# Kernel optimization log

Measured on AMD Instinct MI355X. Metric: run time of the kernel, lower is better.

The kernel has to match this reference:

```python
import jax, jax.numpy as jnp
import numpy as np

N_NODES = 100000
N_EDGES = 3200000
N_GRAPHS = 256
HID = 128


def _glorot(key, shape):
    fan_in = shape[1]
    return jax.random.normal(key, shape, dtype=jnp.float32) / jnp.sqrt(jnp.float32(fan_in))


def setup_inputs() -> dict:
    key = jax.random.key(0)
    ks = jax.random.split(key, 16)
    x = jax.random.normal(ks[0], (N_NODES, 50), dtype=jnp.float32)
    edge_index = jax.random.randint(ks[1], (2, N_EDGES), 0, N_NODES, dtype=jnp.int32)
    batch = jnp.sort(jax.random.randint(ks[2], (N_NODES,), 0, N_GRAPHS, dtype=jnp.int32))
    d1, d2, d3 = HID, HID * 2, HID * 4
    params = {
        'w1l': _glorot(ks[3], (d1, 50)), 'b1': jnp.zeros((d1,), jnp.float32), 'w1r': _glorot(ks[4], (d1, 50)),
        'w2l': _glorot(ks[5], (d2, d1)), 'b2': jnp.zeros((d2,), jnp.float32), 'w2r': _glorot(ks[6], (d2, d1)),
        'w3l': _glorot(ks[7], (d3, d2)), 'b3': jnp.zeros((d3,), jnp.float32), 'w3r': _glorot(ks[8], (d3, d2)),
        'fc1_w': _glorot(ks[9], (d2, d3)), 'fc1_b': jnp.zeros((d2,), jnp.float32),
        'fc2_w': _glorot(ks[10], (d1, d2)), 'fc2_b': jnp.zeros((d1,), jnp.float32),
        'cls_w': _glorot(ks[11], (15, d1)), 'cls_b': jnp.zeros((15,), jnp.float32),
    }
    return {'x': x, 'edge_index': edge_index, 'batch': batch, **params}


def _sage_conv(x, src, dst, wl, b, wr):
    # PyG SAGEConv (mean aggr): out = lin_l(mean_j x_j) + lin_r(x_i)
    agg = jax.ops.segment_sum(x[src], dst, num_segments=N_NODES)
    deg = jax.ops.segment_sum(jnp.ones((src.shape[0],), x.dtype), dst, num_segments=N_NODES)
    agg = agg / jnp.maximum(deg, 1.0)[:, None]
    return agg @ wl.T + b + x @ wr.T


def reference(x, edge_index, batch,
              w1l, b1, w1r, w2l, b2, w2r, w3l, b3, w3r,
              fc1_w, fc1_b, fc2_w, fc2_b, cls_w, cls_b):
    src, dst = edge_index[0], edge_index[1]
    # eval mode: dropout is identity
    h = jax.nn.leaky_relu(_sage_conv(x, src, dst, w1l, b1, w1r), negative_slope=0.01)
    h = jax.nn.relu(_sage_conv(h, src, dst, w2l, b2, w2r))
    h = jax.nn.relu(_sage_conv(h, src, dst, w3l, b3, w3r))
    # global mean pool over graphs
    pooled = jax.ops.segment_sum(h, batch, num_segments=N_GRAPHS)
    cnt = jax.ops.segment_sum(jnp.ones((h.shape[0],), h.dtype), batch, num_segments=N_GRAPHS)
    pooled = pooled / jnp.maximum(cnt, 1.0)[:, None]
    z = jax.nn.relu(pooled @ fc1_w.T + fc1_b)
    z = jax.nn.relu(z @ fc2_w.T + fc2_b)
    return z @ cls_w.T + cls_b
```

## Files before the change

kernel.cpp:

```cpp
#include <hip/hip_runtime.h>
#include <hip/hip_bf16.h>

#define N_NODES 100000
#define N_EDGES 3200000
#define N_GRAPHS 256
#define CAP 80
#define NB 1563
#define NPB 64
#define PBLK 512
#define EPB 6250

typedef __hip_bfloat16 bf16;
using f32x4  = __attribute__((ext_vector_type(4))) float;
using f32x2  = __attribute__((ext_vector_type(2))) float;
using short8 = __attribute__((ext_vector_type(8))) short;

__global__ __launch_bounds__(256) void p1_count(const int* __restrict__ dst,
                                                int* __restrict__ bcount) {
    __shared__ int hist[NB];
    int i = blockIdx.x;
    for (int b = threadIdx.x; b < NB; b += 256) hist[b] = 0;
    __syncthreads();
    int base = i * EPB;
    for (int j = threadIdx.x; j < EPB; j += 256)
        atomicAdd(&hist[dst[base + j] >> 6], 1);
    __syncthreads();
    for (int b = threadIdx.x; b < NB; b += 256) bcount[(size_t)b * PBLK + i] = hist[b];
}

__global__ __launch_bounds__(512) void p2a_total(const int* __restrict__ bcount,
                                                 int* __restrict__ btotal) {
    __shared__ int red[512];
    int b = blockIdx.x;
    red[threadIdx.x] = bcount[(size_t)b * PBLK + threadIdx.x];
    __syncthreads();
    for (int off = 256; off > 0; off >>= 1) {
        if (threadIdx.x < off) red[threadIdx.x] += red[threadIdx.x + off];
        __syncthreads();
    }
    if (threadIdx.x == 0) btotal[b] = red[0];
}

__global__ __launch_bounds__(1024) void p2b_scan(const int* __restrict__ btotal,
                                                 int* __restrict__ bbase) {
    __shared__ int buf[1024];
    __shared__ int carry;
    if (threadIdx.x == 0) carry = 0;
    __syncthreads();
    for (int t = 0; t < NB; t += 1024) {
        int i = t + threadIdx.x;
        int v = (i < NB) ? btotal[i] : 0;
        buf[threadIdx.x] = v;
        __syncthreads();
        for (int off = 1; off < 1024; off <<= 1) {
            int tv = (threadIdx.x >= off) ? buf[threadIdx.x - off] : 0;
            __syncthreads();
            buf[threadIdx.x] += tv;
            __syncthreads();
        }
        if (i < NB) bbase[i] = carry + buf[threadIdx.x] - v;
        __syncthreads();
        if (threadIdx.x == 0) carry += buf[1023];
        __syncthreads();
    }
    if (threadIdx.x == 0) bbase[NB] = carry;
}

__global__ __launch_bounds__(512) void p2c_off(const int* __restrict__ bcount,
                                               const int* __restrict__ bbase,
                                               int* __restrict__ off) {
    __shared__ int buf[512];
    int b = blockIdx.x;
    int v = bcount[(size_t)b * PBLK + threadIdx.x];
    buf[threadIdx.x] = v;
    __syncthreads();
    for (int o = 1; o < 512; o <<= 1) {
        int t = (threadIdx.x >= o) ? buf[threadIdx.x - o] : 0;
        __syncthreads();
        buf[threadIdx.x] += t;
        __syncthreads();
    }
    off[(size_t)threadIdx.x * NB + b] = bbase[b] + buf[threadIdx.x] - v;
}

__global__ __launch_bounds__(256) void p3_scatter(const int* __restrict__ src,
                                                  const int* __restrict__ dst,
                                                  const int* __restrict__ off,
                                                  unsigned int* __restrict__ ebuf) {
    __shared__ int loff[NB];
    int i = blockIdx.x;
    for (int b = threadIdx.x; b < NB; b += 256) loff[b] = off[(size_t)i * NB + b];
    __syncthreads();
    int base = i * EPB;
    for (int j = threadIdx.x; j < EPB; j += 256) {
        int d = dst[base + j];
        int p = atomicAdd(&loff[d >> 6], 1);
        ebuf[p] = ((unsigned)src[base + j] << 6) | (unsigned)(d & 63);
    }
}

__global__ __launch_bounds__(256) void p4_csr(const unsigned int* __restrict__ ebuf,
                                              const int* __restrict__ bbase,
                                              int* __restrict__ cols, int* __restrict__ cnt,
                                              float* __restrict__ invdeg) {
    __shared__ int lcnt[NPB];
    int b = blockIdx.x;
    if (threadIdx.x < NPB) lcnt[threadIdx.x] = 0;
    __syncthreads();
    int s = bbase[b], e = bbase[b + 1];
    int n0 = b * NPB;
    for (int j = s + threadIdx.x; j < e; j += 256) {
        unsigned int p = ebuf[j];
        int dl = p & 63;
        int r = atomicAdd(&lcnt[dl], 1);
        if (r < CAP) cols[(size_t)(n0 + dl) * CAP + r] = (int)(p >> 6);
    }
    __syncthreads();
    if (threadIdx.x < NPB) {
        int n = n0 + threadIdx.x;
        if (n < N_NODES) {
            int c = lcnt[threadIdx.x];
            cnt[n] = c;
            invdeg[n] = 1.0f / fmaxf((float)c, 1.0f);
        }
    }
}

__global__ void xprep_kernel(const float* __restrict__ x, bf16* __restrict__ xb) {
    int t = blockIdx.x * blockDim.x + threadIdx.x;
    if (t >= N_NODES * 64) return;
    int n = t >> 6, f = t & 63;
    xb[t] = __float2bfloat16(f < 50 ? x[(size_t)n * 50 + f] : 0.f);
}

__device__ __forceinline__ void wcvt(const float* __restrict__ s, bf16* __restrict__ d,
                                     int Din, int Kp, int lt) {
    int o = lt / Kp, kk = lt % Kp;
    d[lt] = __float2bfloat16(kk < Din ? s[(size_t)o * Din + kk] : 0.f);
}

__global__ void wprep_all_kernel(const float* w1l, const float* w1r,
                                 const float* w2l, const float* w2r,
                                 const float* w3l, const float* w3r,
                                 bf16* w1l_b, bf16* w1r_b, bf16* w2l_b, bf16* w2r_b,
                                 bf16* w3l_b, bf16* w3r_b) {
    int t = blockIdx.x * blockDim.x + threadIdx.x;
    if      (t < 8192)   wcvt(w1l, w1l_b, 50, 64, t);
    else if (t < 16384)  wcvt(w1r, w1r_b, 50, 64, t - 8192);
    else if (t < 49152)  wcvt(w2l, w2l_b, 128, 128, t - 16384);
    else if (t < 81920)  wcvt(w2r, w2r_b, 128, 128, t - 49152);
    else if (t < 212992) wcvt(w3l, w3l_b, 256, 256, t - 81920);
    else if (t < 344064) wcvt(w3r, w3r_b, 256, 256, t - 212992);
}

template <int D>
__global__ void aggv_kernel(const bf16* __restrict__ h, const int* __restrict__ cnt,
                            const int* __restrict__ cols, const float* __restrict__ invdeg,
                            bf16* __restrict__ AG) {
    constexpr int L = D / 8;
    int n = blockIdx.x * (256 / L) + threadIdx.x / L;
    int lane = threadIdx.x % L;
    if (n >= N_NODES) return;
    const int* cp = cols + (size_t)n * CAP;
    int deg = min(cnt[n], CAP);
    float acc[8] = {};
    auto accum = [&](uint4 v) {
        const unsigned short* u = (const unsigned short*)&v;
#pragma unroll
        for (int i = 0; i < 8; ++i) {
            union { unsigned int ui; float f; } cv;
            cv.ui = ((unsigned int)u[i]) << 16;
            acc[i] += cv.f;
        }
    };
    int j = 0;
    for (; j + 4 <= deg; j += 4) {
        int c0 = cp[j], c1 = cp[j + 1], c2 = cp[j + 2], c3 = cp[j + 3];
        uint4 v0 = *(const uint4*)&h[(size_t)c0 * D + lane * 8];
        uint4 v1 = *(const uint4*)&h[(size_t)c1 * D + lane * 8];
        uint4 v2 = *(const uint4*)&h[(size_t)c2 * D + lane * 8];
        uint4 v3 = *(const uint4*)&h[(size_t)c3 * D + lane * 8];
        accum(v0); accum(v1); accum(v2); accum(v3);
    }
    for (; j < deg; ++j) accum(*(const uint4*)&h[(size_t)cp[j] * D + lane * 8]);
    float inv = invdeg[n];
    union { uint4 u; bf16 h8[8]; } o;
#pragma unroll
    for (int i = 0; i < 8; ++i) o.h8[i] = __float2bfloat16(acc[i] * inv);
    *(uint4*)&AG[(size_t)n * D + lane * 8] = o.u;
}

template <int D>
__global__ void aggv8_kernel(const unsigned char* __restrict__ h8,
                             const int* __restrict__ cnt,
                             const int* __restrict__ cols, const float* __restrict__ invdeg,
                             bf16* __restrict__ AG) {
    constexpr int L = D / 8;
    int n = blockIdx.x * (256 / L) + threadIdx.x / L;
    int lane = threadIdx.x % L;
    if (n >= N_NODES) return;
    const int* cp = cols + (size_t)n * CAP;
    int deg = min(cnt[n], CAP);
    float acc[8] = {};
    auto accum = [&](uint2 v) {
        f32x2 a0 = __builtin_amdgcn_cvt_pk_f32_fp8(v.x, false);
        f32x2 a1 = __builtin_amdgcn_cvt_pk_f32_fp8(v.x, true);
        f32x2 a2 = __builtin_amdgcn_cvt_pk_f32_fp8(v.y, false);
        f32x2 a3 = __builtin_amdgcn_cvt_pk_f32_fp8(v.y, true);
        acc[0] += a0[0]; acc[1] += a0[1]; acc[2] += a1[0]; acc[3] += a1[1];
        acc[4] += a2[0]; acc[5] += a2[1]; acc[6] += a3[0]; acc[7] += a3[1];
    };
    int j = 0;
    for (; j + 8 <= deg; j += 8) {
        uint2 v[8];
#pragma unroll
        for (int q = 0; q < 8; ++q)
            v[q] = *(const uint2*)&h8[(size_t)cp[j + q] * D + lane * 8];
#pragma unroll
        for (int q = 0; q < 8; ++q) accum(v[q]);
    }
    for (; j < deg; ++j) accum(*(const uint2*)&h8[(size_t)cp[j] * D + lane * 8]);
    float inv = invdeg[n];
    union { uint4 u; bf16 hb[8]; } o;
#pragma unroll
    for (int i = 0; i < 8; ++i) o.hb[i] = __float2bfloat16(acc[i] * inv);
    *(uint4*)&AG[(size_t)n * D + lane * 8] = o.u;
}

template <int ACT, int POOL, int OUT8>
__global__ __launch_bounds__(256) void glds_gemm(
        const bf16* __restrict__ A1, const bf16* __restrict__ A2, int Kh,
        const bf16* __restrict__ B1, const bf16* __restrict__ B2,
        const float* __restrict__ bias, bf16* __restrict__ out,
        unsigned char* __restrict__ out8,
        int M, int Dout,
        const int* __restrict__ batch, float* __restrict__ pooled) {
    __shared__ alignas(16) bf16 As[2][128][32];
    __shared__ alignas(16) bf16 Bs[2][128][32];
    __shared__ int sbatch[128];

    const int tid = threadIdx.x;
    const int n0 = blockIdx.y * 128;
    const int o0 = blockIdx.x * 128;

    if (POOL && tid < 128) {
        int n = n0 + tid;
        sbatch[tid] = (n < M) ? batch[n] : -1;
    }

    const int lane = tid & 63;
    const int w = tid >> 6;
    const int wr = w >> 1, wc = w & 1;
    const int lr = lane & 15, hi = lane >> 4;
    const int l4 = lane >> 2;
    const int kc8 = (lane & 3) * 8;

    f32x4 acc[4][4] = {};

    auto stage = [&](int buf, int k0) {
        const bf16* Ap;
        const bf16* Bp;
        int kk;
        if (k0 < Kh) { Ap = A1; Bp = B1; kk = k0; }
        else         { Ap = A2; Bp = B2; kk = k0 - Kh; }
#pragma unroll
        for (int c = 0; c < 2; ++c) {
            int rl = w * 32 + c * 16 + l4;
            size_t ga = (size_t)min(n0 + rl, M - 1) * (size_t)Kh + kk + kc8;
            __builtin_amdgcn_global_load_lds(
                (const __attribute__((address_space(1))) void*)(Ap + ga),
                (__attribute__((address_space(3))) void*)&As[buf][w * 32 + c * 16][0], 16, 0, 0);
            size_t gb = (size_t)(o0 + rl) * (size_t)Kh + kk + kc8;
            __builtin_amdgcn_global_load_lds(
                (const __attribute__((address_space(1))) void*)(Bp + gb),
                (__attribute__((address_space(3))) void*)&Bs[buf][w * 32 + c * 16][0], 16, 0, 0);
        }
    };

    const int nt = (2 * Kh) / 32;
    stage(0, 0);
    asm volatile("s_waitcnt vmcnt(0)\n\ts_barrier" ::: "memory");

    int cur = 0;
    for (int t = 0; t < nt; ++t) {
        if (t + 1 < nt) stage(cur ^ 1, (t + 1) * 32);

        short8 af[4], bfr[4];
#pragma unroll
        for (int m = 0; m < 4; ++m)
            af[m] = *(const short8*)&As[cur][wr * 64 + m * 16 + lr][hi * 8];
#pragma unroll
        for (int n = 0; n < 4; ++n)
            bfr[n] = *(const short8*)&Bs[cur][wc * 64 + n * 16 + lr][hi * 8];
#pragma unroll
        for (int m = 0; m < 4; ++m)
#pragma unroll
            for (int n = 0; n < 4; ++n)
                acc[m][n] = __builtin_amdgcn_mfma_f32_16x16x32_bf16(af[m], bfr[n], acc[m][n], 0, 0, 0);

        if (t + 1 < nt)
            asm volatile("s_waitcnt vmcnt(0)\n\ts_barrier" ::: "memory");
        cur ^= 1;
    }

    float bias_v[4];
#pragma unroll
    for (int n = 0; n < 4; ++n) bias_v[n] = bias[o0 + wc * 64 + n * 16 + lr];

    if (!POOL) {
#pragma unroll
        for (int m = 0; m < 4; ++m) {
#pragma unroll
            for (int j = 0; j < 4; ++j) {
                int row = n0 + wr * 64 + m * 16 + hi * 4 + j;
                if (row < M) {
#pragma unroll
                    for (int n = 0; n < 4; ++n) {
                        int col = o0 + wc * 64 + n * 16 + lr;
                        float s = acc[m][n][j] + bias_v[n];
                        if (ACT == 0) s = (s >= 0.f) ? s : 0.01f * s;
                        else          s = fmaxf(s, 0.f);
                        out[(size_t)row * Dout + col] = __float2bfloat16(s);
                        if (OUT8) {
                            int p = __builtin_amdgcn_cvt_pk_fp8_f32(s, s, 0, false);
                            out8[(size_t)row * Dout + col] = (unsigned char)(p & 0xff);
                        }
                    }
                }
            }
        }
    } else {
        int lastv = min(127, M - 1 - n0);
        int gmin = sbatch[0], gmax = sbatch[lastv];
        for (int g = gmin; g <= gmax; ++g) {
            float s[4] = {0.f, 0.f, 0.f, 0.f};
#pragma unroll
            for (int m = 0; m < 4; ++m) {
#pragma unroll
                for (int j = 0; j < 4; ++j) {
                    int rl = wr * 64 + m * 16 + hi * 4 + j;
                    if (sbatch[rl] == g) {
#pragma unroll
                        for (int n = 0; n < 4; ++n)
                            s[n] += fmaxf(acc[m][n][j] + bias_v[n], 0.f);
                    }
                }
            }
#pragma unroll
            for (int n = 0; n < 4; ++n) {
                float v = s[n];
                v += __shfl_xor(v, 16, 64);
                v += __shfl_xor(v, 32, 64);
                if (hi == 0)
                    atomicAdd(&pooled[(size_t)g * 512 + o0 + wc * 64 + n * 16 + lr], v);
            }
        }
    }
}

__global__ void bounds_kernel(const int* __restrict__ batch, int* __restrict__ gstart) {
    int g = blockIdx.x * blockDim.x + threadIdx.x;
    if (g > N_GRAPHS) return;
    int lo = 0, hi = N_NODES;
    while (lo < hi) {
        int mid = (lo + hi) >> 1;
        if (batch[mid] < g) lo = mid + 1;
        else hi = mid;
    }
    gstart[g] = lo;
}

__global__ void pool_finalize(float* __restrict__ pooled, const int* __restrict__ gstart) {
    int g = blockIdx.x;
    int f = threadIdx.x;
    float cnt = fmaxf((float)(gstart[g + 1] - gstart[g]), 1.0f);
    pooled[(size_t)g * 512 + f] /= cnt;
}

template <int ACT>
__global__ void mlp_kernel(const float* __restrict__ in, const float* __restrict__ w,
                           const float* __restrict__ b, float* __restrict__ out,
                           int M, int K, int O) {
    int t = blockIdx.x * blockDim.x + threadIdx.x;
    if (t >= M * O) return;
    int m = t / O, o = t % O;
    const float* ip = in + (size_t)m * K;
    const float* wp = w + (size_t)o * K;
    float s = 0.f;
    for (int k = 0; k < K; ++k) s += ip[k] * wp[k];
    s += b[o];
    if (ACT) s = fmaxf(s, 0.f);
    out[(size_t)m * O + o] = s;
}

extern "C" void kernel_launch(void* const* d_in, const int* in_sizes, int n_in,
                              void* d_out, int out_size, void* d_ws, size_t ws_size,
                              hipStream_t stream) {
    const float* x     = (const float*)d_in[0];
    const int*   ei    = (const int*)d_in[1];
    const int*   batch = (const int*)d_in[2];
    const float* w1l = (const float*)d_in[3];
    const float* b1  = (const float*)d_in[4];
    const float* w1r = (const float*)d_in[5];
    const float* w2l = (const float*)d_in[6];
    const float* b2  = (const float*)d_in[7];
    const float* w2r = (const float*)d_in[8];
    const float* w3l = (const float*)d_in[9];
    const float* b3  = (const float*)d_in[10];
    const float* w3r = (const float*)d_in[11];
    const float* fc1_w = (const float*)d_in[12];
    const float* fc1_b = (const float*)d_in[13];
    const float* fc2_w = (const float*)d_in[14];
    const float* fc2_b = (const float*)d_in[15];
    const float* cls_w = (const float*)d_in[16];
    const float* cls_b = (const float*)d_in[17];
    float* out = (float*)d_out;

    const int* src = ei;
    const int* dst = ei + N_EDGES;

    char* wsp = (char*)d_ws;
    size_t used = 0;
    auto alloc = [&](size_t bytes) {
        char* p = wsp + used;
        used += (bytes + 255) & ~(size_t)255;
        return p;
    };
    int*   cnt    = (int*)alloc((size_t)N_NODES * 4);
    int*   cols   = (int*)alloc((size_t)N_NODES * CAP * 4);
    float* invdeg = (float*)alloc((size_t)N_NODES * 4);
    int*   gstart = (int*)alloc((size_t)(N_GRAPHS + 1) * 4);
    bf16*  xb     = (bf16*)alloc((size_t)N_NODES * 64 * 2);
    char*  R      = alloc((size_t)N_NODES * 256 * 2);
    bf16*  AG     = (bf16*)R;
    bf16*  h1     = (bf16*)(R + (size_t)N_NODES * 128 * 2);
    bf16*  h2     = (bf16*)alloc((size_t)N_NODES * 256 * 2);
    unsigned char* h1_8 = (unsigned char*)alloc((size_t)N_NODES * 128);
    unsigned char* h2_8 = (unsigned char*)alloc((size_t)N_NODES * 256);
    bf16*  w1l_b  = (bf16*)alloc(128 * 64 * 2);
    bf16*  w1r_b  = (bf16*)alloc(128 * 64 * 2);
    bf16*  w2l_b  = (bf16*)alloc(256 * 128 * 2);
    bf16*  w2r_b  = (bf16*)alloc(256 * 128 * 2);
    bf16*  w3l_b  = (bf16*)alloc(512 * 256 * 2);
    bf16*  w3r_b  = (bf16*)alloc(512 * 256 * 2);
    float* pooled = (float*)alloc((size_t)N_GRAPHS * 512 * 4);
    float* z1     = (float*)alloc((size_t)N_GRAPHS * 256 * 4);
    float* z2     = (float*)alloc((size_t)N_GRAPHS * 128 * 4);

    int* bcount = (int*)h1_8;
    int* btotal = bcount + (size_t)NB * PBLK;
    int* bbase  = btotal + NB;
    int* off    = bbase + NB + 1;
    unsigned int* ebuf = (unsigned int*)h2;

    if (ws_size < used) return;

    p1_count<<<PBLK, 256, 0, stream>>>(dst, bcount);
    p2a_total<<<NB, 512, 0, stream>>>(bcount, btotal);
    p2b_scan<<<1, 1024, 0, stream>>>(btotal, bbase);
    p2c_off<<<NB, 512, 0, stream>>>(bcount, bbase, off);
    p3_scatter<<<PBLK, 256, 0, stream>>>(src, dst, off, ebuf);
    p4_csr<<<NB, 256, 0, stream>>>(ebuf, bbase, cols, cnt, invdeg);
    bounds_kernel<<<2, 160, 0, stream>>>(batch, gstart);

    xprep_kernel<<<(N_NODES * 64 + 255) / 256, 256, 0, stream>>>(x, xb);
    wprep_all_kernel<<<(344064 + 255) / 256, 256, 0, stream>>>(
        w1l, w1r, w2l, w2r, w3l, w3r, w1l_b, w1r_b, w2l_b, w2r_b, w3l_b, w3r_b);

    const int MB = (N_NODES + 127) / 128;

    aggv_kernel<64><<<(N_NODES * 8 + 255) / 256, 256, 0, stream>>>(xb, cnt, cols, invdeg, AG);
    glds_gemm<0, 0, 1><<<dim3(1, MB), 256, 0, stream>>>(
        AG, xb, 64, w1l_b, w1r_b, b1, h1, h1_8, N_NODES, 128, nullptr, nullptr);

    aggv8_kernel<128><<<(N_NODES * 16 + 255) / 256, 256, 0, stream>>>(
        h1_8, cnt, cols, invdeg, AG);
    glds_gemm<1, 0, 1><<<dim3(2, MB), 256, 0, stream>>>(
        AG, h1, 128, w2l_b, w2r_b, b2, h2, h2_8, N_NODES, 256, nullptr, nullptr);

    aggv8_kernel<256><<<(N_NODES * 32 + 255) / 256, 256, 0, stream>>>(
        h2_8, cnt, cols, invdeg, AG);
    hipMemsetAsync(pooled, 0, (size_t)N_GRAPHS * 512 * 4, stream);
    glds_gemm<1, 1, 0><<<dim3(4, MB), 256, 0, stream>>>(
        AG, h2, 256, w3l_b, w3r_b, b3, nullptr, nullptr, N_NODES, 512, batch, pooled);
    pool_finalize<<<N_GRAPHS, 512, 0, stream>>>(pooled, gstart);

    mlp_kernel<1><<<(N_GRAPHS * 256 + 255) / 256, 256, 0, stream>>>(
        pooled, fc1_w, fc1_b, z1, N_GRAPHS, 512, 256);
    mlp_kernel<1><<<(N_GRAPHS * 128 + 255) / 256, 256, 0, stream>>>(
        z1, fc2_w, fc2_b, z2, N_GRAPHS, 256, 128);
    mlp_kernel<0><<<(N_GRAPHS * 15 + 255) / 256, 256, 0, stream>>>(
        z2, cls_w, cls_b, out, N_GRAPHS, 128, 15);
}
```

Measured before the change: 612.0 us.

## Gather layer-1 inputs in fp8, widen aggregation loads, swizzle GEMM tile order

xprep now also writes an fp8 copy of the padded input. Layer-1 aggregation gathers from that copy instead of bf16, so it can use the same fp8 gather kernel as the later layers. The fp8 gather kernel now reads 16 bytes per lane (16 features) instead of 8, halving the threads per node. The GEMM grid is flattened and remapped so groups of 8 row tiles share column tiles, which should help L2 reuse of the A tiles. The risks are extra fp8 quantisation error on the first-layer input and more registers per thread in the gather.

Result: slower. 650.8 us (+6.3%).

```diff
diff --git a/kernel.cpp b/kernel.cpp
--- a/kernel.cpp
+++ b/kernel.cpp
@@ -126,11 +126,15 @@
     }
 }
 
-__global__ void xprep_kernel(const float* __restrict__ x, bf16* __restrict__ xb) {
+__global__ void xprep_kernel(const float* __restrict__ x, bf16* __restrict__ xb,
+                             unsigned char* __restrict__ xb8) {
     int t = blockIdx.x * blockDim.x + threadIdx.x;
     if (t >= N_NODES * 64) return;
     int n = t >> 6, f = t & 63;
-    xb[t] = __float2bfloat16(f < 50 ? x[(size_t)n * 50 + f] : 0.f);
+    float v = (f < 50) ? x[(size_t)n * 50 + f] : 0.f;
+    xb[t] = __float2bfloat16(v);
+    int p = __builtin_amdgcn_cvt_pk_fp8_f32(v, v, 0, false);
+    xb8[t] = (unsigned char)(p & 0xff);
 }
 
 __device__ __forceinline__ void wcvt(const float* __restrict__ s, bf16* __restrict__ d,
@@ -154,80 +158,48 @@
 }
 
 template <int D>
-__global__ void aggv_kernel(const bf16* __restrict__ h, const int* __restrict__ cnt,
-                            const int* __restrict__ cols, const float* __restrict__ invdeg,
-                            bf16* __restrict__ AG) {
-    constexpr int L = D / 8;
+__global__ void aggv8_kernel(const unsigned char* __restrict__ h8,
+                             const int* __restrict__ cnt,
+                             const int* __restrict__ cols, const float* __restrict__ invdeg,
+                             bf16* __restrict__ AG) {
+    constexpr int L = D / 16;
     int n = blockIdx.x * (256 / L) + threadIdx.x / L;
     int lane = threadIdx.x % L;
     if (n >= N_NODES) return;
     const int* cp = cols + (size_t)n * CAP;
     int deg = min(cnt[n], CAP);
-    float acc[8] = {};
+    float acc[16] = {};
     auto accum = [&](uint4 v) {
-        const unsigned short* u = (const unsigned short*)&v;
-#pragma unroll
-        for (int i = 0; i < 8; ++i) {
-            union { unsigned int ui; float f; } cv;
-            cv.ui = ((unsigned int)u[i]) << 16;
-            acc[i] += cv.f;
-        }
-    };
-    int j = 0;
-    for (; j + 4 <= deg; j += 4) {
-        int c0 = cp[j], c1 = cp[j + 1], c2 = cp[j + 2], c3 = cp[j + 3];
-        uint4 v0 = *(const uint4*)&h[(size_t)c0 * D + lane * 8];
-        uint4 v1 = *(const uint4*)&h[(size_t)c1 * D + lane * 8];
-        uint4 v2 = *(const uint4*)&h[(size_t)c2 * D + lane * 8];
-        uint4 v3 = *(const uint4*)&h[(size_t)c3 * D + lane * 8];
-        accum(v0); accum(v1); accum(v2); accum(v3);
-    }
-    for (; j < deg; ++j) accum(*(const uint4*)&h[(size_t)cp[j] * D + lane * 8]);
-    float inv = invdeg[n];
-    union { uint4 u; bf16 h8[8]; } o;
-#pragma unroll
-    for (int i = 0; i < 8; ++i) o.h8[i] = __float2bfloat16(acc[i] * inv);
-    *(uint4*)&AG[(size_t)n * D + lane * 8] = o.u;
-}
-
-template <int D>
-__global__ void aggv8_kernel(const unsigned char* __restrict__ h8,
-                             const int* __restrict__ cnt,
-                             const int* __restrict__ cols, const float* __restrict__ invdeg,
-                             bf16* __restrict__ AG) {
-    constexpr int L = D / 8;
-    int n = blockIdx.x * (256 / L) + threadIdx.x / L;
-    int lane = threadIdx.x % L;
-    if (n >= N_NODES) return;
-    const int* cp = cols + (size_t)n * CAP;
-    int deg = min(cnt[n], CAP);
-    float acc[8] = {};
-    auto accum = [&](uint2 v) {
-        f32x2 a0 = __builtin_amdgcn_cvt_pk_f32_fp8(v.x, false);
-        f32x2 a1 = __builtin_amdgcn_cvt_pk_f32_fp8(v.x, true);
-        f32x2 a2 = __builtin_amdgcn_cvt_pk_f32_fp8(v.y, false);
-        f32x2 a3 = __builtin_amdgcn_cvt_pk_f32_fp8(v.y, true);
-        acc[0] += a0[0]; acc[1] += a0[1]; acc[2] += a1[0]; acc[3] += a1[1];
-        acc[4] += a2[0]; acc[5] += a2[1]; acc[6] += a3[0]; acc[7] += a3[1];
+        unsigned vv[4] = {v.x, v.y, v.z, v.w};
+#pragma unroll
+        for (int q = 0; q < 4; ++q) {
+            f32x2 lo = __builtin_amdgcn_cvt_pk_f32_fp8(vv[q], false);
+            f32x2 hi = __builtin_amdgcn_cvt_pk_f32_fp8(vv[q], true);
+            acc[q * 4 + 0] += lo[0];
+            acc[q * 4 + 1] += lo[1];
+            acc[q * 4 + 2] += hi[0];
+            acc[q * 4 + 3] += hi[1];
+        }
     };
     int j = 0;
     for (; j + 8 <= deg; j += 8) {
-        uint2 v[8];
+        uint4 v[8];
 #pragma unroll
         for (int q = 0; q < 8; ++q)
-            v[q] = *(const uint2*)&h8[(size_t)cp[j + q] * D + lane * 8];
+            v[q] = *(const uint4*)&h8[(size_t)cp[j + q] * D + lane * 16];
 #pragma unroll
         for (int q = 0; q < 8; ++q) accum(v[q]);
     }
-    for (; j < deg; ++j) accum(*(const uint2*)&h8[(size_t)cp[j] * D + lane * 8]);
+    for (; j < deg; ++j) accum(*(const uint4*)&h8[(size_t)cp[j] * D + lane * 16]);
     float inv = invdeg[n];
-    union { uint4 u; bf16 hb[8]; } o;
-#pragma unroll
-    for (int i = 0; i < 8; ++i) o.hb[i] = __float2bfloat16(acc[i] * inv);
-    *(uint4*)&AG[(size_t)n * D + lane * 8] = o.u;
-}
-
-template <int ACT, int POOL, int OUT8>
+    union { uint4 u[2]; bf16 hb[16]; } o;
+#pragma unroll
+    for (int i = 0; i < 16; ++i) o.hb[i] = __float2bfloat16(acc[i] * inv);
+    *(uint4*)&AG[(size_t)n * D + lane * 16] = o.u[0];
+    *(uint4*)&AG[(size_t)n * D + lane * 16 + 8] = o.u[1];
+}
+
+template <int ACT, int POOL, int OUT8, int NX>
 __global__ __launch_bounds__(256) void glds_gemm(
         const bf16* __restrict__ A1, const bf16* __restrict__ A2, int Kh,
         const bf16* __restrict__ B1, const bf16* __restrict__ B2,
@@ -239,9 +211,17 @@
     __shared__ alignas(16) bf16 Bs[2][128][32];
     __shared__ int sbatch[128];
 
+    const int gid = blockIdx.x;
+    const int group = gid / (8 * NX);
+    const int rem = gid % (8 * NX);
+    const int xcol = rem >> 3;
+    const int ytile = group * 8 + (rem & 7);
+    const int MBt = (M + 127) >> 7;
+    if (ytile >= MBt) return;
+
     const int tid = threadIdx.x;
-    const int n0 = blockIdx.y * 128;
-    const int o0 = blockIdx.x * 128;
+    const int n0 = ytile * 128;
+    const int o0 = xcol * 128;
 
     if (POOL && tid < 128) {
         int n = n0 + tid;
@@ -452,6 +432,7 @@
     int* bbase  = btotal + NB;
     int* off    = bbase + NB + 1;
     unsigned int* ebuf = (unsigned int*)h2;
+    unsigned char* xb8 = (unsigned char*)h2;
 
     if (ws_size < used) return;
 
@@ -463,25 +444,26 @@
     p4_csr<<<NB, 256, 0, stream>>>(ebuf, bbase, cols, cnt, invdeg);
     bounds_kernel<<<2, 160, 0, stream>>>(batch, gstart);
 
-    xprep_kernel<<<(N_NODES * 64 + 255) / 256, 256, 0, stream>>>(x, xb);
+    xprep_kernel<<<(N_NODES * 64 + 255) / 256, 256, 0, stream>>>(x, xb, xb8);
     wprep_all_kernel<<<(344064 + 255) / 256, 256, 0, stream>>>(
         w1l, w1r, w2l, w2r, w3l, w3r, w1l_b, w1r_b, w2l_b, w2r_b, w3l_b, w3r_b);
 
-    const int MB = (N_NODES + 127) / 128;
-
-    aggv_kernel<64><<<(N_NODES * 8 + 255) / 256, 256, 0, stream>>>(xb, cnt, cols, invdeg, AG);
-    glds_gemm<0, 0, 1><<<dim3(1, MB), 256, 0, stream>>>(
+    const int GB = 98 * 8;
+
+    aggv8_kernel<64><<<(N_NODES * 4 + 255) / 256, 256, 0, stream>>>(
+        xb8, cnt, cols, invdeg, AG);
+    glds_gemm<0, 0, 1, 1><<<GB, 256, 0, stream>>>(
         AG, xb, 64, w1l_b, w1r_b, b1, h1, h1_8, N_NODES, 128, nullptr, nullptr);
 
-    aggv8_kernel<128><<<(N_NODES * 16 + 255) / 256, 256, 0, stream>>>(
+    aggv8_kernel<128><<<(N_NODES * 8 + 255) / 256, 256, 0, stream>>>(
         h1_8, cnt, cols, invdeg, AG);
-    glds_gemm<1, 0, 1><<<dim3(2, MB), 256, 0, stream>>>(
+    glds_gemm<1, 0, 1, 2><<<GB * 2, 256, 0, stream>>>(
         AG, h1, 128, w2l_b, w2r_b, b2, h2, h2_8, N_NODES, 256, nullptr, nullptr);
 
-    aggv8_kernel<256><<<(N_NODES * 32 + 255) / 256, 256, 0, stream>>>(
+    aggv8_kernel<256><<<(N_NODES * 16 + 255) / 256, 256, 0, stream>>>(
         h2_8, cnt, cols, invdeg, AG);
     hipMemsetAsync(pooled, 0, (size_t)N_GRAPHS * 512 * 4, stream);
-    glds_gemm<1, 1, 0><<<dim3(4, MB), 256, 0, stream>>>(
+    glds_gemm<1, 1, 0, 4><<<GB * 4, 256, 0, stream>>>(
         AG, h2, 256, w3l_b, w3r_b, b3, nullptr, nullptr, N_NODES, 512, batch, pooled);
     pool_finalize<<<N_GRAPHS, 512, 0, stream>>>(pooled, gstart);
 
```
